# Kernel optimization log

Hardware: AMD Instinct MI355X
Metric: run time of the kernel (lower is better)

Reference implementation:

```python
import jax, jax.numpy as jnp
import numpy as np

BN_EPS = 1e-5
LRELU_SLOPE = 0.2
N_NODES, N_EDGES, D_IN, D_OUT = 20000, 320000, 256, 256


def _leaky(h):
    return jnp.where(h >= 0, h, LRELU_SLOPE * h)


def _bn_eval(h, gamma, beta):
    # BatchNorm1d in eval mode with running_mean=0, running_var=1
    return gamma * (h / jnp.sqrt(1.0 + BN_EPS)) + beta


def setup_inputs() -> dict:
    key = jax.random.key(0)
    ks = jax.random.split(key, 16)
    inp = {
        "x": jax.random.normal(ks[0], (N_NODES, D_IN), jnp.float32),
        "pos": jax.random.normal(ks[1], (N_NODES, 3), jnp.float32),
        "edge_index": jax.random.randint(ks[2], (2, N_EDGES), 0, N_NODES, jnp.int32),
        # node projection (nn.Linear(D_IN, D_OUT)), stored as (in, out)
        "Wn_w": jax.random.normal(ks[3], (D_IN, D_OUT), jnp.float32) * (1.0 / np.sqrt(D_IN)),
        "Wn_b": jnp.zeros((D_OUT,), jnp.float32),
        # distance MLP: 1 -> 256 -> 512 -> 256 -> 1 with BN(gamma,beta) after first 3 linears
        "w1": jax.random.normal(ks[4], (1, 256), jnp.float32),
        "b1": jnp.zeros((256,), jnp.float32),
        "g1": jnp.ones((256,), jnp.float32),
        "be1": jnp.zeros((256,), jnp.float32),
        "w2": jax.random.normal(ks[5], (256, 512), jnp.float32) * (1.0 / np.sqrt(256)),
        "b2": jnp.zeros((512,), jnp.float32),
        "g2": jnp.ones((512,), jnp.float32),
        "be2": jnp.zeros((512,), jnp.float32),
        "w3": jax.random.normal(ks[6], (512, 256), jnp.float32) * (1.0 / np.sqrt(512)),
        "b3": jnp.zeros((256,), jnp.float32),
        "g3": jnp.ones((256,), jnp.float32),
        "be3": jnp.zeros((256,), jnp.float32),
        "w4": jax.random.normal(ks[7], (256, 1), jnp.float32) * (1.0 / np.sqrt(256)),
        "b4": jnp.zeros((1,), jnp.float32),
    }
    return inp


def reference(x, pos, edge_index, Wn_w, Wn_b, w1, b1, g1, be1, w2, b2, g2, be2, w3, b3, g3, be3, w4, b4):
    row, col = edge_index[0], edge_index[1]
    n = x.shape[0]

    # per-edge L2 distance, [E, 1]
    diff = pos[row] - pos[col]
    dist = jnp.sqrt(jnp.sum(diff * diff, axis=-1, keepdims=True))

    # distance embedding MLP (BN eval, dropout off) -> [E, 1]
    h = _leaky(_bn_eval(dist @ w1 + b1, g1, be1))
    h = _leaky(_bn_eval(h @ w2 + b2, g2, be2))
    h = _leaky(_bn_eval(h @ w3 + b3, g3, be3))
    emb = h @ w4 + b4

    # node projection
    x_proj = x @ Wn_w + Wn_b  # [N, D_OUT]

    # symmetric-normalized adjacency coefficient per edge (degree from row only, as in source)
    ones = jnp.ones((row.shape[0],), x.dtype)
    deg = jax.ops.segment_sum(ones, row, num_segments=n)
    deg = jnp.where(deg == 0, 1.0, deg)
    dinv = deg ** -0.5
    norm = dinv[row] * dinv[col]  # [E]

    w = norm[:, None] * emb  # [E, 1]

    # symmetric gather-scale-scatter: each edge contributes both directions
    aggr = jax.ops.segment_sum(w * x_proj[col], row, num_segments=n)
    aggr = aggr + jax.ops.segment_sum(w * x_proj[row], col, num_segments=n)

    return jnp.concatenate([jax.nn.relu(aggr), pos], axis=-1)  # [N, D_OUT + 3]
```

## Files before the change

### kernel.cpp

```cpp
#include <hip/hip_runtime.h>
#include <math.h>

constexpr int TBL_N = 512;
constexpr float TBL_RANGE = 16.0f;
constexpr int MAXDEG = 80;
constexpr int TB_TBL = TBL_N / 16;
constexpr int H1PAD = 264;
constexpr int H2PAD = 520;
constexpr int NXCD = 8;
constexpr float XQS = 16.0f;

typedef __attribute__((ext_vector_type(8))) short short8;
typedef __attribute__((ext_vector_type(4))) float f32x4;

__device__ __forceinline__ unsigned short f2bf(float f) {
    unsigned int u = __float_as_uint(f);
    u = (u + 0x7fffu + ((u >> 16) & 1u)) >> 16;
    return (unsigned short)u;
}
__device__ __forceinline__ float bflo(unsigned int u) { return __uint_as_float(u << 16); }
__device__ __forceinline__ float bfhi(unsigned int u) { return __uint_as_float(u & 0xffff0000u); }

__device__ __forceinline__ unsigned short h1q(float d, float w, float b, float gs, float e) {
    float z = fmaf(gs, fmaf(d, w, b), e);
    z = z >= 0.f ? z : 0.2f * z;
    return f2bf(z);
}
__device__ __forceinline__ unsigned int pk4(float4 v) {
    int q0 = __float2int_rn(v.x * XQS), q1 = __float2int_rn(v.y * XQS);
    int q2 = __float2int_rn(v.z * XQS), q3 = __float2int_rn(v.w * XQS);
    return ((unsigned)q0 & 0xffu) | (((unsigned)q1 & 0xffu) << 8) |
           (((unsigned)q2 & 0xffu) << 16) | (((unsigned)q3 & 0xffu) << 24);
}
__device__ __forceinline__ void cvt8i(const float4* src, uint2* dst, int i8) {
    float4 a = src[i8 * 2], b = src[i8 * 2 + 1];
    uint2 o; o.x = pk4(a); o.y = pk4(b);
    dst[i8] = o;
}

__global__ __launch_bounds__(256) void k_phase1(
    const int* __restrict__ ei, int E, int n,
    const float* __restrict__ x, unsigned char* __restrict__ xb,
    const float* __restrict__ Wn_w, unsigned short* __restrict__ Wt,
    const float* __restrict__ pos,
    unsigned int* __restrict__ pc, unsigned int* __restrict__ adj,
    const float* __restrict__ w1, const float* __restrict__ b1,
    const float* __restrict__ g1, const float* __restrict__ be1,
    const float* __restrict__ w2, const float* __restrict__ b2,
    const float* __restrict__ g2, const float* __restrict__ be2,
    const float* __restrict__ w3, const float* __restrict__ b3,
    const float* __restrict__ g3, const float* __restrict__ be3,
    const float* __restrict__ w4, const float* __restrict__ b4,
    float* __restrict__ table) {
    __shared__ __align__(16) char smem[25600];
    __shared__ int qn;
    const int t = threadIdx.x;
    const int DCH = (E + 1023) >> 10;
    const int B0 = DCH * NXCD;
    int b = blockIdx.x;

    if (b < TB_TBL) {
        auto h1s = (unsigned short (*)[H1PAD])smem;
        auto h2s = (unsigned short (*)[H2PAD])(smem + 16 * H1PAD * 2);
        auto red = (float (*)[16])(smem + 16 * H1PAD * 2 + 16 * H2PAD * 2);
        const int w = t >> 6, lane = t & 63, r = lane & 15, g = lane >> 4;
        const float inv_s = 1.0f / sqrtf(1.0f + 1e-5f);
        const float hstep = TBL_RANGE / (float)(TBL_N - 1);
        const int srow0 = b * 16;

        {
            const int row = t >> 4, c0 = (t & 15) * 16;
            const float d = (float)(srow0 + row) * hstep;
            #pragma unroll
            for (int c = 0; c < 16; c += 4) {
                float4 wv = *(const float4*)&w1[c0 + c];
                float4 bv = *(const float4*)&b1[c0 + c];
                float4 gv = *(const float4*)&g1[c0 + c];
                float4 ev = *(const float4*)&be1[c0 + c];
                ushort4 o;
                o.x = h1q(d, wv.x, bv.x, gv.x * inv_s, ev.x);
                o.y = h1q(d, wv.y, bv.y, gv.y * inv_s, ev.y);
                o.z = h1q(d, wv.z, bv.z, gv.z * inv_s, ev.z);
                o.w = h1q(d, wv.w, bv.w, gv.w * inv_s, ev.w);
                *(ushort4*)&h1s[row][c0 + c] = o;
            }
        }
        __syncthreads();

        f32x4 acc1[8] = {};
        #pragma unroll
        for (int kt = 0; kt < 8; ++kt) {
            const int k0 = kt * 32 + g * 8;
            short8 a = *(const short8*)&h1s[r][k0];
            #pragma unroll
            for (int j = 0; j < 8; ++j) {
                const int nn = w * 128 + j * 16 + r;
                short8 bfr;
                #pragma unroll
                for (int kk = 0; kk < 8; ++kk)
                    bfr[kk] = (short)f2bf(w2[(size_t)(k0 + kk) * 512 + nn]);
                acc1[j] = __builtin_amdgcn_mfma_f32_16x16x32_bf16(a, bfr, acc1[j], 0, 0, 0);
            }
        }
        #pragma unroll
        for (int j = 0; j < 8; ++j) {
            const int nn = w * 128 + j * 16 + r;
            float gaa = g2[nn] * inv_s, bbb = b2[nn], bee = be2[nn];
            #pragma unroll
            for (int i = 0; i < 4; ++i) {
                float z = fmaf(gaa, acc1[j][i] + bbb, bee);
                z = z >= 0.f ? z : 0.2f * z;
                h2s[g * 4 + i][nn] = f2bf(z);
            }
        }
        __syncthreads();

        f32x4 acc2[4] = {};
        #pragma unroll
        for (int kt = 0; kt < 16; ++kt) {
            const int k0 = kt * 32 + g * 8;
            short8 a2 = *(const short8*)&h2s[r][k0];
            #pragma unroll
            for (int j = 0; j < 4; ++j) {
                const int nn = w * 64 + j * 16 + r;
                short8 bfr;
                #pragma unroll
                for (int kk = 0; kk < 8; ++kk)
                    bfr[kk] = (short)f2bf(w3[(size_t)(k0 + kk) * 256 + nn]);
                acc2[j] = __builtin_amdgcn_mfma_f32_16x16x32_bf16(a2, bfr, acc2[j], 0, 0, 0);
            }
        }
        float vsum[4] = {};
        #pragma unroll
        for (int j = 0; j < 4; ++j) {
            const int nn = w * 64 + j * 16 + r;
            float gaa = g3[nn] * inv_s, bbb = b3[nn], bee = be3[nn], w4v = w4[nn];
            #pragma unroll
            for (int i = 0; i < 4; ++i) {
                float z = fmaf(gaa, acc2[j][i] + bbb, bee);
                z = z >= 0.f ? z : 0.2f * z;
                vsum[i] = fmaf(z, w4v, vsum[i]);
            }
        }
        #pragma unroll
        for (int off = 1; off < 16; off <<= 1) {
            #pragma unroll
            for (int i = 0; i < 4; ++i) vsum[i] += __shfl_xor(vsum[i], off);
        }
        if (r == 0) {
            #pragma unroll
            for (int i = 0; i < 4; ++i) red[w][g * 4 + i] = vsum[i];
        }
        __syncthreads();
        if (t < 16) table[srow0 + t] = red[0][t] + red[1][t] + red[2][t] + red[3][t] + b4[0];
        return;
    }
    b -= TB_TBL;

    if (b < 256) {
        auto tile = (float (*)[33])smem;
        const int r0 = (b % 8) << 5, c0 = (b / 8) << 5;
        const int tx = t & 31, ty = t >> 5;
        #pragma unroll
        for (int i = 0; i < 4; ++i)
            tile[ty + 8 * i][tx] = Wn_w[(size_t)(r0 + ty + 8 * i) * 256 + c0 + tx];
        __syncthreads();
        #pragma unroll
        for (int i = 0; i < 4; ++i)
            Wt[(size_t)(c0 + ty + 8 * i) * 256 + r0 + tx] = f2bf(tile[tx][ty + 8 * i]);
        return;
    }
    b -= 256;

    if (b < B0) {
        auto q = (unsigned int*)smem;
        const int range = b & 7, chunk = b >> 3;
        const int base = n >> 3;
        const int lo = range * base, sz = (range == 7) ? (n - 7 * base) : base;
        if (t == 0) qn = 0;
        __syncthreads();
        int e0 = chunk * 1024 + t * 4;
        if (e0 + 3 < E) {
            int4 r4 = *(const int4*)&ei[e0];
            int4 c4 = *(const int4*)&ei[E + e0];
            int rr[4] = {r4.x, r4.y, r4.z, r4.w};
            int cc[4] = {c4.x, c4.y, c4.z, c4.w};
            #pragma unroll
            for (int k = 0; k < 4; ++k) {
                int r = rr[k], c = cc[k];
                if ((unsigned)(r - lo) < (unsigned)sz) {
                    int p = atomicAdd(&qn, 1);
                    q[p] = 0x40000000u | ((unsigned)r << 15) | (unsigned)c;
                }
                if ((unsigned)(c - lo) < (unsigned)sz) {
                    int p = atomicAdd(&qn, 1);
                    q[p] = ((unsigned)c << 15) | (unsigned)r;
                }
            }
        } else {
            for (int e = e0; e < E; ++e) {
                int r = ei[e], c = ei[E + e];
                if ((unsigned)(r - lo) < (unsigned)sz) {
                    int p = atomicAdd(&qn, 1);
                    q[p] = 0x40000000u | ((unsigned)r << 15) | (unsigned)c;
                }
                if ((unsigned)(c - lo) < (unsigned)sz) {
                    int p = atomicAdd(&qn, 1);
                    q[p] = ((unsigned)c << 15) | (unsigned)r;
                }
            }
        }
        __syncthreads();
        const int m = qn;
        for (int p = t; p < m; p += 256) {
            unsigned int ent = q[p];
            int tgt = (int)((ent >> 15) & 0x7fffu);
            int nbr = (int)(ent & 0x7fffu);
            float3 pa = *(const float3*)&pos[tgt * 3];
            float3 pb = *(const float3*)&pos[nbr * 3];
            float dx = pa.x - pb.x, dy = pa.y - pb.y, dz = pa.z - pb.z;
            float dist = sqrtf(dx * dx + dy * dy + dz * dz);
            float u = fminf(dist * ((float)(TBL_N - 1) / TBL_RANGE), (float)(TBL_N - 1));
            unsigned int ud = (unsigned int)(u * 16.0f + 0.5f);
            unsigned int inc = (ent & 0x40000000u) ? 0x10001u : 1u;
            unsigned int old = atomicAdd(&pc[tgt], inc);
            int s = (int)(old & 0xffffu);
            if (s < MAXDEG) adj[(size_t)tgt * MAXDEG + s] = ((unsigned int)nbr << 16) | ud;
        }
        return;
    }
    b -= B0;

    int i8 = b * 256 + t;
    cvt8i((const float4*)x, (uint2*)xb, i8);
}

__global__ __launch_bounds__(1024) void k_gatherproj(
    const unsigned char* __restrict__ xb, const unsigned short* __restrict__ Wt,
    const float* __restrict__ bias, const float* __restrict__ pos,
    const float* __restrict__ table,
    const unsigned int* __restrict__ pc, const unsigned int* __restrict__ adj,
    float* __restrict__ out, int n) {
    __shared__ unsigned short agg[16][H1PAD];
    __shared__ unsigned int wlds[16][MAXDEG];
    __shared__ float wsl[16];
    const int t = threadIdx.x;
    const int w = t >> 6, lane = t & 63;
    const int node0 = blockIdx.x * 16;
    const int node = node0 + w;

    unsigned int pcv = pc[node];
    int m = (int)(pcv & 0xffffu); if (m > MAXDEG) m = MAXDEG;
    {
        int dg = (int)(pcv >> 16);
        const float din = dg ? rsqrtf((float)dg) : 1.0f;
        const unsigned int* a = adj + (size_t)node * MAXDEG;
        #pragma unroll
        for (int s = lane; s < MAXDEG; s += 64) {
            unsigned int o = 0;
            if (s < m) {
                unsigned int e = a[s];
                int nbr = min((int)(e >> 16), n - 1);
                unsigned int pcn = pc[nbr];
                int dgn = (int)(pcn >> 16);
                float dn = dgn ? rsqrtf((float)dgn) : 1.0f;
                float u = (float)(e & 0xffffu) * (1.0f / 16.0f);
                int i = min((int)u, TBL_N - 2);
                float f = u - (float)i;
                float t0 = table[i], t1 = table[i + 1];
                float wv = din * dn * fmaf(f, t1 - t0, t0);
                o = ((unsigned int)nbr << 16) | f2bf(wv);
            }
            wlds[w][s] = o;
        }
    }
    __syncthreads();

    {
        const int m8 = (m + 7) & ~7;
        float4 acc = make_float4(0.f, 0.f, 0.f, 0.f);
        float ws = 0.f;
        for (int p = 0; p < m8; p += 8) {
            uint4 A = *(const uint4*)&wlds[w][p];
            uint4 B = *(const uint4*)&wlds[w][p + 4];
            unsigned int en[8] = {A.x, A.y, A.z, A.w, B.x, B.y, B.z, B.w};
            unsigned int v[8];
            #pragma unroll
            for (int k = 0; k < 8; ++k)
                v[k] = *(const unsigned int*)&xb[(size_t)(en[k] >> 16) * 256 + lane * 4];
            #pragma unroll
            for (int k = 0; k < 8; ++k) {
                float wv = bflo(en[k]);
                ws += wv;
                acc.x = fmaf(wv, (float)(signed char)(v[k]), acc.x);
                acc.y = fmaf(wv, (float)(signed char)(v[k] >> 8), acc.y);
                acc.z = fmaf(wv, (float)(signed char)(v[k] >> 16), acc.z);
                acc.w = fmaf(wv, (float)(signed char)(v[k] >> 24), acc.w);
            }
        }
        ushort4 o;
        o.x = f2bf(acc.x * (1.0f / XQS)); o.y = f2bf(acc.y * (1.0f / XQS));
        o.z = f2bf(acc.z * (1.0f / XQS)); o.w = f2bf(acc.w * (1.0f / XQS));
        *(ushort4*)&agg[w][lane * 4] = o;
        if (lane == 0) wsl[w] = ws;
    }
    __syncthreads();

    if (w < 4) {
        const int r = lane & 15, g = lane >> 4;
        f32x4 acc[4] = {};
        #pragma unroll
        for (int kt = 0; kt < 8; ++kt) {
            const int k0 = kt * 32 + g * 8;
            short8 afr = *(const short8*)&agg[r][k0];
            #pragma unroll
            for (int j = 0; j < 4; ++j) {
                short8 bfr = *(const short8*)&Wt[(size_t)(w * 64 + j * 16 + r) * 256 + k0];
                acc[j] = __builtin_amdgcn_mfma_f32_16x16x32_bf16(afr, bfr, acc[j], 0, 0, 0);
            }
        }
        #pragma unroll
        for (int j = 0; j < 4; ++j) {
            const int col = w * 64 + j * 16 + r;
            const float bv = bias[col];
            #pragma unroll
            for (int i = 0; i < 4; ++i) {
                const int nl = g * 4 + i;
                float val = acc[j][i] + wsl[nl] * bv;
                out[(size_t)(node0 + nl) * 259 + col] = fmaxf(val, 0.f);
            }
        }
    }
    if (t < 48) {
        const int nl = t / 3, c = t % 3;
        out[(size_t)(node0 + nl) * 259 + 256 + c] = pos[(node0 + nl) * 3 + c];
    }
}

extern "C" void kernel_launch(void* const* d_in, const int* in_sizes, int n_in,
                              void* d_out, int out_size, void* d_ws, size_t ws_size,
                              hipStream_t stream) {
    (void)n_in; (void)out_size; (void)ws_size;
    const float* x    = (const float*)d_in[0];
    const float* pos  = (const float*)d_in[1];
    const int*   ei   = (const int*)d_in[2];
    const float* Wn_w = (const float*)d_in[3];
    const float* Wn_b = (const float*)d_in[4];
    const float* w1 = (const float*)d_in[5];
    const float* b1 = (const float*)d_in[6];
    const float* g1 = (const float*)d_in[7];
    const float* be1 = (const float*)d_in[8];
    const float* w2 = (const float*)d_in[9];
    const float* b2 = (const float*)d_in[10];
    const float* g2 = (const float*)d_in[11];
    const float* be2 = (const float*)d_in[12];
    const float* w3 = (const float*)d_in[13];
    const float* b3 = (const float*)d_in[14];
    const float* g3 = (const float*)d_in[15];
    const float* be3 = (const float*)d_in[16];
    const float* w4 = (const float*)d_in[17];
    const float* b4 = (const float*)d_in[18];
    float* out = (float*)d_out;

    const int n = in_sizes[1] / 3;
    const int E = in_sizes[2] / 2;

    char* ws = (char*)d_ws;
    unsigned int* pc    = (unsigned int*)(ws + 0);
    float* table        = (float*)(ws + 81920);
    unsigned int* adj   = (unsigned int*)(ws + 98304);
    unsigned short* Wt  = (unsigned short*)(ws + 6498304);
    unsigned char* xb   = (unsigned char*)(ws + 6629376);

    hipMemsetAsync(ws, 0, 81920, stream);

    const int DCH = (E + 1023) >> 10;
    const int B_p1 = TB_TBL + 256 + DCH * NXCD + (n >> 3);

    k_phase1<<<B_p1, 256, 0, stream>>>(ei, E, n, x, xb, Wn_w, Wt, pos, pc, adj,
                                       w1, b1, g1, be1, w2, b2, g2, be2,
                                       w3, b3, g3, be3, w4, b4, table);
    k_gatherproj<<<n / 16, 1024, 0, stream>>>(xb, Wt, Wn_b, pos, table, pc, adj, out, n);
}
```

Baseline: 90.24 us.

## Split table MLP hidden layer into halves, unroll adjacency fill, replace memset kernel

The distance-table MLP now computes the first hidden layer in registers and processes the 512-wide second layer in two 256-column halves, accumulating the third layer across halves. This cuts the shared memory per block from about 25 KB to under 9 KB, which applies to every phase1 block and so can raise occupancy. The adjacency-building loop now handles two queue entries per iteration so more gathers and atomics are in flight at once. The hipMemsetAsync is replaced by a small zeroing kernel that clears only n counters. The trade-off is an extra block barrier and recomputing h1 from global parameters in each pass.

```diff
diff --git a/kernel.cpp b/kernel.cpp
--- a/kernel.cpp
+++ b/kernel.cpp
@@ -6,7 +6,7 @@
 constexpr int MAXDEG = 80;
 constexpr int TB_TBL = TBL_N / 16;
 constexpr int H1PAD = 264;
-constexpr int H2PAD = 520;
+constexpr int H2HALF = 264;
 constexpr int NXCD = 8;
 constexpr float XQS = 16.0f;
 
@@ -19,7 +19,6 @@
     return (unsigned short)u;
 }
 __device__ __forceinline__ float bflo(unsigned int u) { return __uint_as_float(u << 16); }
-__device__ __forceinline__ float bfhi(unsigned int u) { return __uint_as_float(u & 0xffff0000u); }
 
 __device__ __forceinline__ unsigned short h1q(float d, float w, float b, float gs, float e) {
     float z = fmaf(gs, fmaf(d, w, b), e);
@@ -36,6 +35,11 @@
     float4 a = src[i8 * 2], b = src[i8 * 2 + 1];
     uint2 o; o.x = pk4(a); o.y = pk4(b);
     dst[i8] = o;
+}
+
+__global__ __launch_bounds__(256) void k_zero(uint4* __restrict__ p, int n4) {
+    int i = blockIdx.x * 256 + threadIdx.x;
+    if (i < n4) p[i] = make_uint4(0, 0, 0, 0);
 }
 
 __global__ __launch_bounds__(256) void k_phase1(
@@ -52,7 +56,7 @@
     const float* __restrict__ g3, const float* __restrict__ be3,
     const float* __restrict__ w4, const float* __restrict__ b4,
     float* __restrict__ table) {
-    __shared__ __align__(16) char smem[25600];
+    __shared__ __align__(16) char smem[8704];
     __shared__ int qn;
     const int t = threadIdx.x;
     const int DCH = (E + 1023) >> 10;
@@ -60,74 +64,63 @@
     int b = blockIdx.x;
 
     if (b < TB_TBL) {
-        auto h1s = (unsigned short (*)[H1PAD])smem;
-        auto h2s = (unsigned short (*)[H2PAD])(smem + 16 * H1PAD * 2);
-        auto red = (float (*)[16])(smem + 16 * H1PAD * 2 + 16 * H2PAD * 2);
+        auto h2s = (unsigned short (*)[H2HALF])smem;
+        auto red = (float (*)[16])(smem + 16 * H2HALF * 2);
         const int w = t >> 6, lane = t & 63, r = lane & 15, g = lane >> 4;
         const float inv_s = 1.0f / sqrtf(1.0f + 1e-5f);
         const float hstep = TBL_RANGE / (float)(TBL_N - 1);
         const int srow0 = b * 16;
-
-        {
-            const int row = t >> 4, c0 = (t & 15) * 16;
-            const float d = (float)(srow0 + row) * hstep;
-            #pragma unroll
-            for (int c = 0; c < 16; c += 4) {
-                float4 wv = *(const float4*)&w1[c0 + c];
-                float4 bv = *(const float4*)&b1[c0 + c];
-                float4 gv = *(const float4*)&g1[c0 + c];
-                float4 ev = *(const float4*)&be1[c0 + c];
-                ushort4 o;
-                o.x = h1q(d, wv.x, bv.x, gv.x * inv_s, ev.x);
-                o.y = h1q(d, wv.y, bv.y, gv.y * inv_s, ev.y);
-                o.z = h1q(d, wv.z, bv.z, gv.z * inv_s, ev.z);
-                o.w = h1q(d, wv.w, bv.w, gv.w * inv_s, ev.w);
-                *(ushort4*)&h1s[row][c0 + c] = o;
-            }
-        }
-        __syncthreads();
-
-        f32x4 acc1[8] = {};
-        #pragma unroll
-        for (int kt = 0; kt < 8; ++kt) {
-            const int k0 = kt * 32 + g * 8;
-            short8 a = *(const short8*)&h1s[r][k0];
-            #pragma unroll
-            for (int j = 0; j < 8; ++j) {
-                const int nn = w * 128 + j * 16 + r;
-                short8 bfr;
+        const float d = (float)(srow0 + r) * hstep;
+
+        f32x4 acc2[4] = {};
+        #pragma unroll
+        for (int h = 0; h < 2; ++h) {
+            f32x4 acc1[4] = {};
+            #pragma unroll
+            for (int kt = 0; kt < 8; ++kt) {
+                const int k0 = kt * 32 + g * 8;
+                short8 a;
                 #pragma unroll
                 for (int kk = 0; kk < 8; ++kk)
-                    bfr[kk] = (short)f2bf(w2[(size_t)(k0 + kk) * 512 + nn]);
-                acc1[j] = __builtin_amdgcn_mfma_f32_16x16x32_bf16(a, bfr, acc1[j], 0, 0, 0);
-            }
-        }
-        #pragma unroll
-        for (int j = 0; j < 8; ++j) {
-            const int nn = w * 128 + j * 16 + r;
-            float gaa = g2[nn] * inv_s, bbb = b2[nn], bee = be2[nn];
-            #pragma unroll
-            for (int i = 0; i < 4; ++i) {
-                float z = fmaf(gaa, acc1[j][i] + bbb, bee);
-                z = z >= 0.f ? z : 0.2f * z;
-                h2s[g * 4 + i][nn] = f2bf(z);
-            }
-        }
-        __syncthreads();
-
-        f32x4 acc2[4] = {};
-        #pragma unroll
-        for (int kt = 0; kt < 16; ++kt) {
-            const int k0 = kt * 32 + g * 8;
-            short8 a2 = *(const short8*)&h2s[r][k0];
+                    a[kk] = (short)h1q(d, w1[k0 + kk], b1[k0 + kk],
+                                       g1[k0 + kk] * inv_s, be1[k0 + kk]);
+                #pragma unroll
+                for (int j = 0; j < 4; ++j) {
+                    const int nn = h * 256 + w * 64 + j * 16 + r;
+                    short8 bfr;
+                    #pragma unroll
+                    for (int kk = 0; kk < 8; ++kk)
+                        bfr[kk] = (short)f2bf(w2[(size_t)(k0 + kk) * 512 + nn]);
+                    acc1[j] = __builtin_amdgcn_mfma_f32_16x16x32_bf16(a, bfr, acc1[j], 0, 0, 0);
+                }
+            }
+            __syncthreads();
             #pragma unroll
             for (int j = 0; j < 4; ++j) {
-                const int nn = w * 64 + j * 16 + r;
-                short8 bfr;
+                const int nl = w * 64 + j * 16 + r;
+                const int nn = h * 256 + nl;
+                float gaa = g2[nn] * inv_s, bbb = b2[nn], bee = be2[nn];
                 #pragma unroll
-                for (int kk = 0; kk < 8; ++kk)
-                    bfr[kk] = (short)f2bf(w3[(size_t)(k0 + kk) * 256 + nn]);
-                acc2[j] = __builtin_amdgcn_mfma_f32_16x16x32_bf16(a2, bfr, acc2[j], 0, 0, 0);
+                for (int i = 0; i < 4; ++i) {
+                    float z = fmaf(gaa, acc1[j][i] + bbb, bee);
+                    z = z >= 0.f ? z : 0.2f * z;
+                    h2s[g * 4 + i][nl] = f2bf(z);
+                }
+            }
+            __syncthreads();
+            #pragma unroll
+            for (int kt = 0; kt < 8; ++kt) {
+                const int k0 = kt * 32 + g * 8;
+                short8 a2 = *(const short8*)&h2s[r][k0];
+                #pragma unroll
+                for (int j = 0; j < 4; ++j) {
+                    const int nn2 = w * 64 + j * 16 + r;
+                    short8 bfr;
+                    #pragma unroll
+                    for (int kk = 0; kk < 8; ++kk)
+                        bfr[kk] = (short)f2bf(w3[(size_t)(h * 256 + k0 + kk) * 256 + nn2]);
+                    acc2[j] = __builtin_amdgcn_mfma_f32_16x16x32_bf16(a2, bfr, acc2[j], 0, 0, 0);
+                }
             }
         }
         float vsum[4] = {};
@@ -212,20 +205,34 @@
         }
         __syncthreads();
         const int m = qn;
-        for (int p = t; p < m; p += 256) {
-            unsigned int ent = q[p];
-            int tgt = (int)((ent >> 15) & 0x7fffu);
-            int nbr = (int)(ent & 0x7fffu);
-            float3 pa = *(const float3*)&pos[tgt * 3];
-            float3 pb = *(const float3*)&pos[nbr * 3];
-            float dx = pa.x - pb.x, dy = pa.y - pb.y, dz = pa.z - pb.z;
-            float dist = sqrtf(dx * dx + dy * dy + dz * dz);
-            float u = fminf(dist * ((float)(TBL_N - 1) / TBL_RANGE), (float)(TBL_N - 1));
-            unsigned int ud = (unsigned int)(u * 16.0f + 0.5f);
-            unsigned int inc = (ent & 0x40000000u) ? 0x10001u : 1u;
-            unsigned int old = atomicAdd(&pc[tgt], inc);
-            int s = (int)(old & 0xffffu);
-            if (s < MAXDEG) adj[(size_t)tgt * MAXDEG + s] = ((unsigned int)nbr << 16) | ud;
+        for (int p = t; p < m; p += 512) {
+            unsigned int ea = q[p];
+            bool h1v = (p + 256) < m;
+            unsigned int eb = h1v ? q[p + 256] : ea;
+            int tg0 = (int)((ea >> 15) & 0x7fffu), nb0 = (int)(ea & 0x7fffu);
+            int tg1 = (int)((eb >> 15) & 0x7fffu), nb1 = (int)(eb & 0x7fffu);
+            float3 pa0 = *(const float3*)&pos[tg0 * 3];
+            float3 pb0 = *(const float3*)&pos[nb0 * 3];
+            float3 pa1 = *(const float3*)&pos[tg1 * 3];
+            float3 pb1 = *(const float3*)&pos[nb1 * 3];
+            float dx0 = pa0.x - pb0.x, dy0 = pa0.y - pb0.y, dz0 = pa0.z - pb0.z;
+            float dx1 = pa1.x - pb1.x, dy1 = pa1.y - pb1.y, dz1 = pa1.z - pb1.z;
+            float u0 = fminf(sqrtf(dx0 * dx0 + dy0 * dy0 + dz0 * dz0) *
+                             ((float)(TBL_N - 1) / TBL_RANGE), (float)(TBL_N - 1));
+            float u1 = fminf(sqrtf(dx1 * dx1 + dy1 * dy1 + dz1 * dz1) *
+                             ((float)(TBL_N - 1) / TBL_RANGE), (float)(TBL_N - 1));
+            unsigned int ud0 = (unsigned int)(u0 * 16.0f + 0.5f);
+            unsigned int ud1 = (unsigned int)(u1 * 16.0f + 0.5f);
+            unsigned int in0 = (ea & 0x40000000u) ? 0x10001u : 1u;
+            unsigned int in1 = (eb & 0x40000000u) ? 0x10001u : 1u;
+            unsigned int o0 = atomicAdd(&pc[tg0], in0);
+            unsigned int o1 = h1v ? atomicAdd(&pc[tg1], in1) : 0u;
+            int s0 = (int)(o0 & 0xffffu);
+            if (s0 < MAXDEG) adj[(size_t)tg0 * MAXDEG + s0] = ((unsigned int)nb0 << 16) | ud0;
+            if (h1v) {
+                int s1 = (int)(o1 & 0xffffu);
+                if (s1 < MAXDEG) adj[(size_t)tg1 * MAXDEG + s1] = ((unsigned int)nb1 << 16) | ud1;
+            }
         }
         return;
     }
@@ -372,11 +379,10 @@
     unsigned short* Wt  = (unsigned short*)(ws + 6498304);
     unsigned char* xb   = (unsigned char*)(ws + 6629376);
 
-    hipMemsetAsync(ws, 0, 81920, stream);
-
     const int DCH = (E + 1023) >> 10;
     const int B_p1 = TB_TBL + 256 + DCH * NXCD + (n >> 3);
 
+    k_zero<<<(n / 4 + 255) / 256, 256, 0, stream>>>((uint4*)pc, n / 4);
     k_phase1<<<B_p1, 256, 0, stream>>>(ei, E, n, x, xb, Wn_w, Wt, pos, pc, adj,
                                        w1, b1, g1, be1, w2, b2, g2, be2,
                                        w3, b3, g3, be3, w4, b4, table);
```

After: 155.3 us. 1.72x slower.
